# Kernel optimization log

Hardware: AMD Instinct MI355X
Metric: run time of the kernel (lower is better)

Reference implementation:

```python
import jax, jax.numpy as jnp
import numpy as np

NUM_HEADS = 16
WINDOW_SIZE = 256  # config.window_size; layer is 'local'


def setup_inputs() -> dict:
    key = jax.random.key(0)
    ks = jax.random.split(key, 8)
    B, S, H = 4, 2048, 1024
    scale = 1.0 / np.sqrt(H)
    return {
        "x": jax.random.normal(ks[0], (B, S, H), dtype=jnp.float32),
        "x_clean": jax.random.normal(ks[1], (B, S, H), dtype=jnp.float32),
        "ablation_mask": jax.random.uniform(ks[2], (B, S, H), dtype=jnp.float32),
        "Wq": jax.random.normal(ks[3], (H, H), dtype=jnp.float32) * scale,
        "Wk": jax.random.normal(ks[4], (H, H), dtype=jnp.float32) * scale,
        "Wv": jax.random.normal(ks[5], (H, H), dtype=jnp.float32) * scale,
        "Wo": jax.random.normal(ks[6], (H, H), dtype=jnp.float32) * scale,
        "bo": jnp.zeros((H,), dtype=jnp.float32),
    }


def reference(x, x_clean, ablation_mask, Wq, Wk, Wv, Wo, bo):
    B, S, H = x.shape
    nh, hd = NUM_HEADS, H // NUM_HEADS

    def proj(inp, W):  # torch Linear: inp @ W.T -> split heads -> [B, nh, S, hd]
        return jnp.einsum('bsh,oh->bso', inp, W).reshape(B, S, nh, hd).transpose(0, 2, 1, 3)

    q = proj(x, Wq)
    k = proj(x_clean, Wk)
    v = proj(x_clean, Wv)

    # NOTE: original applies NO 1/sqrt(head_dim) scaling.
    scores = jnp.einsum('bnsd,bntd->bnst', q, k)  # [B, nh, S, S]

    i = jnp.arange(S)[:, None]
    j = jnp.arange(S)[None, :]
    # local mask: forbid future (j > i) OR too-far past (j <= i - window)
    masked = (j > i) | (j <= i - WINDOW_SIZE)
    scores = jnp.where(masked[None, None, :, :], -jnp.inf, scores)

    attn = jax.nn.softmax(scores, axis=-1)
    context = jnp.einsum('bnst,bntd->bnsd', attn, v)          # [B, nh, S, hd]
    context = context.transpose(0, 2, 1, 3).reshape(B, S, H)   # merge heads
    context = context * ablation_mask
    return jnp.einsum('bsh,oh->bso', context, Wo) + bo
```

## Files before the change

### kernel.cpp

```cpp
#include <hip/hip_runtime.h>
#include <hip/hip_bf16.h>
#include <cstddef>

#define SB 4
#define SS 2048
#define SH 1024
#define NH 16
#define HD 64
#define WIN 256

typedef __attribute__((ext_vector_type(8))) short bf16x8;
typedef __attribute__((ext_vector_type(8))) _Float16 f16x8;
typedef __attribute__((ext_vector_type(2))) __fp16 fp16v2;
typedef __attribute__((ext_vector_type(4))) float f32x4;

static __device__ __forceinline__ ushort2 pk_bf16(float a, float b) {
    __hip_bfloat162 h = __float22bfloat162_rn(make_float2(a, b));
    union { __hip_bfloat162 h2; ushort2 u2; } u;
    u.h2 = h;
    return u.u2;
}
static __device__ __forceinline__ unsigned short pk1(float a) {
    return pk_bf16(a, 0.f).x;
}

static __device__ __forceinline__ void async16(const void* gptr, void* lptr) {
    __builtin_amdgcn_global_load_lds(
        (const __attribute__((address_space(1))) unsigned int*)gptr,
        (__attribute__((address_space(3))) unsigned int*)lptr, 16, 0, 0);
}

__global__ __launch_bounds__(256) void cvt_all(
    const float* __restrict__ x,  const float* __restrict__ xc,
    const float* __restrict__ Wq, const float* __restrict__ Wk,
    const float* __restrict__ Wv, const float* __restrict__ Wo,
    _Float16* __restrict__ xh,  _Float16* __restrict__ xch,
    _Float16* __restrict__ Wqh, _Float16* __restrict__ Wkh,
    _Float16* __restrict__ Wvh, _Float16* __restrict__ Woh)
{
    const int I4 = SB * SS * SH / 4;
    const int W4 = SH * SH / 4;
    int idx = blockIdx.x * 256 + threadIdx.x;
    const float* src;
    _Float16* dst;
    int off;
    if (idx < I4) { src = x; dst = xh; off = idx; }
    else if (idx < 2 * I4) { src = xc; dst = xch; off = idx - I4; }
    else {
        int r = idx - 2 * I4;
        int wi = r >> 18;
        off = r & (W4 - 1);
        src = (wi == 0) ? Wq : (wi == 1) ? Wk : (wi == 2) ? Wv : Wo;
        dst = (wi == 0) ? Wqh : (wi == 1) ? Wkh : (wi == 2) ? Wvh : Woh;
    }
    float4 v = ((const float4*)src)[off];
    union { fp16v2 h[2]; uint2 u; } t;
    t.h[0] = __builtin_amdgcn_cvt_pkrtz(v.x, v.y);
    t.h[1] = __builtin_amdgcn_cvt_pkrtz(v.z, v.w);
    ((uint2*)dst)[off] = t.u;
}

template<int OUTM>
__global__ __launch_bounds__(256) void gemm5(
    const _Float16* __restrict__ A, const _Float16* __restrict__ W,
    const float* __restrict__ bias, void* __restrict__ C1v,
    int M, int N, int K)
{
    __shared__ __align__(16) unsigned short smem[2 * 128 * 64];
    _Float16* Ah = (_Float16*)smem;
    _Float16* Bh = (_Float16*)smem + 8192;

    const int tid = threadIdx.x;
    const int m0 = blockIdx.x * 128;
    const int n0 = blockIdx.y * 128;
    const int wave = tid >> 6;
    const int lane = tid & 63;
    const int wm = (wave & 1) * 64;
    const int wn = (wave >> 1) * 64;
    const int lrow = lane & 15;
    const int lk8 = (lane >> 4) * 8;
    const int rq = (lane >> 4) * 4;

    f32x4 acc[4][4];
#pragma unroll
    for (int i = 0; i < 4; ++i)
#pragma unroll
        for (int j = 0; j < 4; ++j)
            acc[i][j] = (f32x4){0.f, 0.f, 0.f, 0.f};

    for (int k0 = 0; k0 < K; k0 += 64) {
        __syncthreads();
#pragma unroll
        for (int ki = 0; ki < 2; ++ki)
#pragma unroll
            for (int u = 0; u < 2; ++u) {
                int reg = u * 4 + wave;
                int slot = reg * 64 + lane;
                int row = slot >> 2;
                int k8 = (slot & 3) * 8;
                async16(A + (size_t)(m0 + row) * K + k0 + ki * 32 + k8,
                        Ah + ki * 4096 + reg * 512);
                async16(W + (size_t)(n0 + row) * K + k0 + ki * 32 + k8,
                        Bh + ki * 4096 + reg * 512);
            }
        __syncthreads();

#pragma unroll
        for (int ki = 0; ki < 2; ++ki) {
            f16x8 bf[4];
#pragma unroll
            for (int j = 0; j < 4; ++j)
                bf[j] = *(const f16x8*)&Bh[ki * 4096 + (wn + j * 16 + lrow) * 32 + lk8];
#pragma unroll
            for (int i = 0; i < 4; ++i) {
                f16x8 af = *(const f16x8*)&Ah[ki * 4096 + (wm + i * 16 + lrow) * 32 + lk8];
#pragma unroll
                for (int j = 0; j < 4; ++j)
                    acc[i][j] = __builtin_amdgcn_mfma_f32_16x16x32_f16(af, bf[j], acc[i][j], 0, 0, 0);
            }
        }
    }

    if (OUTM == 0) {
        float* C = (float*)C1v;
#pragma unroll
        for (int i = 0; i < 4; ++i) {
            int rbase = m0 + wm + i * 16 + rq;
#pragma unroll
            for (int j = 0; j < 4; ++j) {
                int col = n0 + wn + j * 16 + lrow;
                float badd = bias[col];
#pragma unroll
                for (int r = 0; r < 4; ++r)
                    C[(size_t)(rbase + r) * N + col] = acc[i][j][r] + badd;
            }
        }
    } else if (OUTM == 1) {
        _Float16* C = (_Float16*)C1v;
#pragma unroll
        for (int i = 0; i < 4; ++i) {
            int rbase = m0 + wm + i * 16 + rq;
#pragma unroll
            for (int j = 0; j < 4; ++j) {
                int col = n0 + wn + j * 16 + lrow;
#pragma unroll
                for (int r = 0; r < 4; ++r)
                    C[(size_t)(rbase + r) * N + col] = (_Float16)acc[i][j][r];
            }
        }
    } else {
        unsigned short* Ct = (unsigned short*)C1v;
        unsigned short* T = smem;
#pragma unroll
        for (int p = 0; p < 2; ++p) {
            __syncthreads();
            if (wn == p * 64) {
#pragma unroll
                for (int i = 0; i < 4; ++i) {
                    int mloc = wm + i * 16 + rq;
#pragma unroll
                    for (int j = 0; j < 4; ++j) {
                        int cl = j * 16 + lrow;
                        *(ushort4*)&T[cl * 136 + mloc] = make_ushort4(
                            pk1(acc[i][j][0]), pk1(acc[i][j][1]),
                            pk1(acc[i][j][2]), pk1(acc[i][j][3]));
                    }
                }
            }
            __syncthreads();
#pragma unroll
            for (int u = 0; u < 4; ++u) {
                int slot = u * 256 + tid;
                int cl = slot >> 4;
                int m8 = (slot & 15) * 8;
                *(uint4*)(Ct + (size_t)(n0 + p * 64 + cl) * M + m0 + m8) =
                    *(const uint4*)&T[cl * 136 + m8];
            }
        }
    }
}

__global__ __launch_bounds__(128) void attn3(
    const _Float16* Qg, const _Float16* __restrict__ Kg,
    const unsigned short* __restrict__ Vtg, const float* __restrict__ amask,
    _Float16* ctxg)
{
    __shared__ __align__(16) unsigned short P_s[2][32 * 72];

    const int t = threadIdx.x;
    const int wave = t >> 6, lane = t & 63;
    const int h = blockIdx.y, b = blockIdx.z;
    const int wq = blockIdx.x * 64 + wave * 32;
    const int lrow = lane & 15;
    const int lk8 = (lane >> 4) * 8;
    const int rq = (lane >> 4) * 4;
    const int M = SB * SS;
    unsigned short* P = P_s[wave];

    f16x8 qf[2][2];
#pragma unroll
    for (int i = 0; i < 2; ++i)
#pragma unroll
        for (int ki = 0; ki < 2; ++ki)
            qf[i][ki] = *(const f16x8*)(Qg +
                (size_t)(b * SS + wq + i * 16 + lrow) * SH + h * HD + ki * 32 + lk8);

    f32x4 o[2][4];
    float lsum[2][4];
#pragma unroll
    for (int i = 0; i < 2; ++i)
#pragma unroll
        for (int j = 0; j < 4; ++j) o[i][j] = (f32x4){0.f, 0.f, 0.f, 0.f};
#pragma unroll
    for (int i = 0; i < 2; ++i)
#pragma unroll
        for (int r = 0; r < 4; ++r) lsum[i][r] = 0.f;

    int cl = wq - (WIN - 1);
    cl = cl < 0 ? 0 : cl;
    const int c_lo = cl >> 6;
    const int c_hi = (wq + 31) >> 6;

    for (int c = c_lo; c <= c_hi; ++c) {
        const int key0 = c * 64;

        f16x8 kf[2][4];
#pragma unroll
        for (int ki = 0; ki < 2; ++ki)
#pragma unroll
            for (int j = 0; j < 4; ++j)
                kf[ki][j] = *(const f16x8*)(Kg +
                    (size_t)(b * SS + key0 + j * 16 + lrow) * SH + h * HD + ki * 32 + lk8);

        f32x4 s[2][4];
#pragma unroll
        for (int i = 0; i < 2; ++i)
#pragma unroll
            for (int j = 0; j < 4; ++j) s[i][j] = (f32x4){0.f, 0.f, 0.f, 0.f};
#pragma unroll
        for (int ki = 0; ki < 2; ++ki)
#pragma unroll
            for (int j = 0; j < 4; ++j)
#pragma unroll
                for (int i = 0; i < 2; ++i)
                    s[i][j] = __builtin_amdgcn_mfma_f32_16x16x32_f16(qf[i][ki], kf[ki][j], s[i][j], 0, 0, 0);

#pragma unroll
        for (int i = 0; i < 2; ++i)
#pragma unroll
            for (int j = 0; j < 4; ++j) {
                int jg = key0 + j * 16 + lrow;
#pragma unroll
                for (int r = 0; r < 4; ++r) {
                    int qg = wq + i * 16 + rq + r;
                    float p = (jg <= qg && jg > qg - WIN) ? __expf(s[i][j][r]) : 0.f;
                    lsum[i][r] += p;
                    P[(i * 16 + rq + r) * 72 + j * 16 + lrow] = pk1(p);
                }
            }

        bf16x8 vf[2][4];
#pragma unroll
        for (int ki = 0; ki < 2; ++ki)
#pragma unroll
            for (int j = 0; j < 4; ++j)
                vf[ki][j] = *(const bf16x8*)(Vtg +
                    (size_t)(h * HD + j * 16 + lrow) * M + b * SS + key0 + ki * 32 + lk8);

#pragma unroll
        for (int ki = 0; ki < 2; ++ki) {
            bf16x8 pf[2];
#pragma unroll
            for (int i = 0; i < 2; ++i)
                pf[i] = *(const bf16x8*)&P[(i * 16 + lrow) * 72 + ki * 32 + lk8];
#pragma unroll
            for (int j = 0; j < 4; ++j)
#pragma unroll
                for (int i = 0; i < 2; ++i)
                    o[i][j] = __builtin_amdgcn_mfma_f32_16x16x32_bf16(pf[i], vf[ki][j], o[i][j], 0, 0, 0);
        }
    }

#pragma unroll
    for (int i = 0; i < 2; ++i)
#pragma unroll
        for (int r = 0; r < 4; ++r) {
#pragma unroll
            for (int m = 1; m < 16; m <<= 1)
                lsum[i][r] += __shfl_xor(lsum[i][r], m);
        }

    _Float16* Pf = (_Float16*)P;
#pragma unroll
    for (int i = 0; i < 2; ++i)
#pragma unroll
        for (int r = 0; r < 4; ++r) {
            float inv = 1.f / lsum[i][r];
#pragma unroll
            for (int j = 0; j < 4; ++j)
                Pf[(i * 16 + rq + r) * 72 + j * 16 + lrow] = (_Float16)(o[i][j][r] * inv);
        }
#pragma unroll
    for (int u = 0; u < 4; ++u) {
        int slot = u * 64 + lane;
        int ro = slot >> 3;
        int d8 = (slot & 7) * 8;
        f16x8 v = *(const f16x8*)&Pf[ro * 72 + d8];
        size_t g = (size_t)(b * SS + wq + ro) * SH + h * HD + d8;
        float4 ma = *(const float4*)(amask + g);
        float4 mb = *(const float4*)(amask + g + 4);
        f16x8 rs;
        rs[0] = (_Float16)((float)v[0] * ma.x);
        rs[1] = (_Float16)((float)v[1] * ma.y);
        rs[2] = (_Float16)((float)v[2] * ma.z);
        rs[3] = (_Float16)((float)v[3] * ma.w);
        rs[4] = (_Float16)((float)v[4] * mb.x);
        rs[5] = (_Float16)((float)v[5] * mb.y);
        rs[6] = (_Float16)((float)v[6] * mb.z);
        rs[7] = (_Float16)((float)v[7] * mb.w);
        *(f16x8*)(ctxg + g) = rs;
    }
}

extern "C" void kernel_launch(void* const* d_in, const int* in_sizes, int n_in,
                              void* d_out, int out_size, void* d_ws, size_t ws_size,
                              hipStream_t stream)
{
    const float* x     = (const float*)d_in[0];
    const float* xc    = (const float*)d_in[1];
    const float* amask = (const float*)d_in[2];
    const float* Wq    = (const float*)d_in[3];
    const float* Wk    = (const float*)d_in[4];
    const float* Wv    = (const float*)d_in[5];
    const float* Wo    = (const float*)d_in[6];
    const float* bo    = (const float*)d_in[7];
    float* out = (float*)d_out;

    const int M = SB * SS;
    const size_t BUF = (size_t)M * SH;
    const size_t WBUF = (size_t)SH * SH;
    _Float16* xh  = (_Float16*)d_ws;
    _Float16* xch = xh + BUF;
    _Float16* Qh  = xch + BUF;
    _Float16* Kh  = Qh + BUF;
    unsigned short* Vt = (unsigned short*)(Kh + BUF);
    _Float16* Wqh = (_Float16*)(Vt + BUF);
    _Float16* Wkh = Wqh + WBUF;
    _Float16* Wvh = Wkh + WBUF;
    _Float16* Woh = Wvh + WBUF;
    _Float16* ctx = Qh;

    const int total4 = 2 * (M * SH / 4) + 4 * (SH * SH / 4);
    hipLaunchKernelGGL(cvt_all, dim3(total4 / 256), dim3(256), 0, stream,
                       x, xc, Wq, Wk, Wv, Wo, xh, xch, Wqh, Wkh, Wvh, Woh);

    dim3 gg(M / 128, SH / 128);
    dim3 gb(256);
    hipLaunchKernelGGL((gemm5<1>), gg, gb, 0, stream, xh,  Wqh, bo, (void*)Qh, M, SH, SH);
    hipLaunchKernelGGL((gemm5<1>), gg, gb, 0, stream, xch, Wkh, bo, (void*)Kh, M, SH, SH);
    hipLaunchKernelGGL((gemm5<2>), gg, gb, 0, stream, xch, Wvh, bo, (void*)Vt, M, SH, SH);

    hipLaunchKernelGGL(attn3, dim3(SS / 64, NH, SB), dim3(128), 0, stream,
                       Qh, Kh, Vt, amask, ctx);

    hipLaunchKernelGGL((gemm5<0>), gg, gb, 0, stream, ctx, Woh, bo, (void*)out, M, SH, SH);
}
```

Measured before the change: 304.4 us.

## Merge QKV projections into one launch and stage K/V tiles through shared memory

The three Q/K/V projection GEMMs become a single launch that uses blockIdx.z to pick inputs and outputs. This removes two launch gaps and lets the three projections share the GPU in one wave. The attention kernel grows to 4 waves covering 128 queries per block, and K and V chunks are loaded with async copies into double-buffered shared memory, so the waves share them instead of each wave reading them from global memory. Each wave skips chunks outside its window, but the per-chunk __syncthreads adds synchronisation, and the larger blocks mean fewer blocks in the grid.

```diff
diff --git a/kernel.cpp b/kernel.cpp
--- a/kernel.cpp
+++ b/kernel.cpp
@@ -60,15 +60,21 @@
     ((uint2*)dst)[off] = t.u;
 }
 
-template<int OUTM>
-__global__ __launch_bounds__(256) void gemm5(
-    const _Float16* __restrict__ A, const _Float16* __restrict__ W,
-    const float* __restrict__ bias, void* __restrict__ C1v,
-    int M, int N, int K)
+__global__ __launch_bounds__(256) void gemm_qkv(
+    const _Float16* __restrict__ xh, const _Float16* __restrict__ xch,
+    const _Float16* __restrict__ Wqh, const _Float16* __restrict__ Wkh,
+    const _Float16* __restrict__ Wvh,
+    _Float16* __restrict__ Qh, _Float16* __restrict__ Kh,
+    unsigned short* __restrict__ Vt)
 {
+    const int M = SB * SS, N = SH, K = SH;
     __shared__ __align__(16) unsigned short smem[2 * 128 * 64];
     _Float16* Ah = (_Float16*)smem;
     _Float16* Bh = (_Float16*)smem + 8192;
+
+    const int z = blockIdx.z;
+    const _Float16* A = (z == 0) ? xh : xch;
+    const _Float16* W = (z == 0) ? Wqh : (z == 1) ? Wkh : Wvh;
 
     const int tid = threadIdx.x;
     const int m0 = blockIdx.x * 128;
@@ -121,35 +127,20 @@
         }
     }
 
-    if (OUTM == 0) {
-        float* C = (float*)C1v;
+    if (z < 2) {
+        _Float16* C = (z == 0) ? Qh : Kh;
 #pragma unroll
         for (int i = 0; i < 4; ++i) {
             int rbase = m0 + wm + i * 16 + rq;
 #pragma unroll
             for (int j = 0; j < 4; ++j) {
                 int col = n0 + wn + j * 16 + lrow;
-                float badd = bias[col];
-#pragma unroll
-                for (int r = 0; r < 4; ++r)
-                    C[(size_t)(rbase + r) * N + col] = acc[i][j][r] + badd;
-            }
-        }
-    } else if (OUTM == 1) {
-        _Float16* C = (_Float16*)C1v;
-#pragma unroll
-        for (int i = 0; i < 4; ++i) {
-            int rbase = m0 + wm + i * 16 + rq;
-#pragma unroll
-            for (int j = 0; j < 4; ++j) {
-                int col = n0 + wn + j * 16 + lrow;
 #pragma unroll
                 for (int r = 0; r < 4; ++r)
                     C[(size_t)(rbase + r) * N + col] = (_Float16)acc[i][j][r];
             }
         }
     } else {
-        unsigned short* Ct = (unsigned short*)C1v;
         unsigned short* T = smem;
 #pragma unroll
         for (int p = 0; p < 2; ++p) {
@@ -173,24 +164,101 @@
                 int slot = u * 256 + tid;
                 int cl = slot >> 4;
                 int m8 = (slot & 15) * 8;
-                *(uint4*)(Ct + (size_t)(n0 + p * 64 + cl) * M + m0 + m8) =
+                *(uint4*)(Vt + (size_t)(n0 + p * 64 + cl) * M + m0 + m8) =
                     *(const uint4*)&T[cl * 136 + m8];
             }
         }
     }
 }
 
-__global__ __launch_bounds__(128) void attn3(
+__global__ __launch_bounds__(256) void gemm_o(
+    const _Float16* __restrict__ A, const _Float16* __restrict__ W,
+    const float* __restrict__ bias, float* __restrict__ C)
+{
+    const int M = SB * SS, N = SH, K = SH;
+    __shared__ __align__(16) unsigned short smem[2 * 128 * 64];
+    _Float16* Ah = (_Float16*)smem;
+    _Float16* Bh = (_Float16*)smem + 8192;
+
+    const int tid = threadIdx.x;
+    const int m0 = blockIdx.x * 128;
+    const int n0 = blockIdx.y * 128;
+    const int wave = tid >> 6;
+    const int lane = tid & 63;
+    const int wm = (wave & 1) * 64;
+    const int wn = (wave >> 1) * 64;
+    const int lrow = lane & 15;
+    const int lk8 = (lane >> 4) * 8;
+    const int rq = (lane >> 4) * 4;
+
+    f32x4 acc[4][4];
+#pragma unroll
+    for (int i = 0; i < 4; ++i)
+#pragma unroll
+        for (int j = 0; j < 4; ++j)
+            acc[i][j] = (f32x4){0.f, 0.f, 0.f, 0.f};
+
+    for (int k0 = 0; k0 < K; k0 += 64) {
+        __syncthreads();
+#pragma unroll
+        for (int ki = 0; ki < 2; ++ki)
+#pragma unroll
+            for (int u = 0; u < 2; ++u) {
+                int reg = u * 4 + wave;
+                int slot = reg * 64 + lane;
+                int row = slot >> 2;
+                int k8 = (slot & 3) * 8;
+                async16(A + (size_t)(m0 + row) * K + k0 + ki * 32 + k8,
+                        Ah + ki * 4096 + reg * 512);
+                async16(W + (size_t)(n0 + row) * K + k0 + ki * 32 + k8,
+                        Bh + ki * 4096 + reg * 512);
+            }
+        __syncthreads();
+
+#pragma unroll
+        for (int ki = 0; ki < 2; ++ki) {
+            f16x8 bf[4];
+#pragma unroll
+            for (int j = 0; j < 4; ++j)
+                bf[j] = *(const f16x8*)&Bh[ki * 4096 + (wn + j * 16 + lrow) * 32 + lk8];
+#pragma unroll
+            for (int i = 0; i < 4; ++i) {
+                f16x8 af = *(const f16x8*)&Ah[ki * 4096 + (wm + i * 16 + lrow) * 32 + lk8];
+#pragma unroll
+                for (int j = 0; j < 4; ++j)
+                    acc[i][j] = __builtin_amdgcn_mfma_f32_16x16x32_f16(af, bf[j], acc[i][j], 0, 0, 0);
+            }
+        }
+    }
+
+#pragma unroll
+    for (int i = 0; i < 4; ++i) {
+        int rbase = m0 + wm + i * 16 + rq;
+#pragma unroll
+        for (int j = 0; j < 4; ++j) {
+            int col = n0 + wn + j * 16 + lrow;
+            float badd = bias[col];
+#pragma unroll
+            for (int r = 0; r < 4; ++r)
+                C[(size_t)(rbase + r) * N + col] = acc[i][j][r] + badd;
+        }
+    }
+}
+
+__global__ __launch_bounds__(256) void attn4(
     const _Float16* Qg, const _Float16* __restrict__ Kg,
     const unsigned short* __restrict__ Vtg, const float* __restrict__ amask,
     _Float16* ctxg)
 {
-    __shared__ __align__(16) unsigned short P_s[2][32 * 72];
+    __shared__ __align__(16) _Float16 K_s[2][2 * 64 * 32];
+    __shared__ __align__(16) unsigned short V_s[2][2 * 64 * 32];
+    __shared__ __align__(16) unsigned short P_s[4][32 * 72];
 
     const int t = threadIdx.x;
     const int wave = t >> 6, lane = t & 63;
-    const int h = blockIdx.y, b = blockIdx.z;
-    const int wq = blockIdx.x * 64 + wave * 32;
+    const int qb = blockIdx.x, h = blockIdx.y, b = blockIdx.z;
+    const int t0 = qb * 128;
+    const int wq = t0 + wave * 32;
     const int lrow = lane & 15;
     const int lk8 = (lane >> 4) * 8;
     const int rq = (lane >> 4) * 4;
@@ -216,69 +284,81 @@
 #pragma unroll
         for (int r = 0; r < 4; ++r) lsum[i][r] = 0.f;
 
-    int cl = wq - (WIN - 1);
-    cl = cl < 0 ? 0 : cl;
-    const int c_lo = cl >> 6;
-    const int c_hi = (wq + 31) >> 6;
+    int cl0 = t0 - (WIN - 1);
+    cl0 = cl0 < 0 ? 0 : cl0;
+    const int c_lo = cl0 >> 6;
+    const int c_hi = (t0 >> 6) + 1;
+
+    auto stage = [&](int c, int buf) {
+        const int key0 = c * 64;
+#pragma unroll
+        for (int ki = 0; ki < 2; ++ki) {
+            int slot = wave * 64 + lane;
+            int row = slot >> 2;
+            int e8 = (slot & 3) * 8;
+            async16(Kg + (size_t)(b * SS + key0 + row) * SH + h * HD + ki * 32 + e8,
+                    (_Float16*)K_s[buf] + ki * 2048 + wave * 512);
+            async16(Vtg + (size_t)(h * HD + row) * M + b * SS + key0 + ki * 32 + e8,
+                    (unsigned short*)V_s[buf] + ki * 2048 + wave * 512);
+        }
+    };
+
+    stage(c_lo, c_lo & 1);
+    __syncthreads();
 
     for (int c = c_lo; c <= c_hi; ++c) {
+        const int cur = c & 1;
+        if (c < c_hi) stage(c + 1, cur ^ 1);
         const int key0 = c * 64;
-
-        f16x8 kf[2][4];
-#pragma unroll
-        for (int ki = 0; ki < 2; ++ki)
-#pragma unroll
-            for (int j = 0; j < 4; ++j)
-                kf[ki][j] = *(const f16x8*)(Kg +
-                    (size_t)(b * SS + key0 + j * 16 + lrow) * SH + h * HD + ki * 32 + lk8);
-
-        f32x4 s[2][4];
-#pragma unroll
-        for (int i = 0; i < 2; ++i)
-#pragma unroll
-            for (int j = 0; j < 4; ++j) s[i][j] = (f32x4){0.f, 0.f, 0.f, 0.f};
-#pragma unroll
-        for (int ki = 0; ki < 2; ++ki)
-#pragma unroll
-            for (int j = 0; j < 4; ++j)
+        if (key0 <= wq + 31 && key0 + 63 >= wq - (WIN - 1)) {
+            const _Float16* Kc = (const _Float16*)K_s[cur];
+            const unsigned short* Vc = (const unsigned short*)V_s[cur];
+
+            f32x4 s[2][4];
+#pragma unroll
+            for (int i = 0; i < 2; ++i)
+#pragma unroll
+                for (int j = 0; j < 4; ++j) s[i][j] = (f32x4){0.f, 0.f, 0.f, 0.f};
+#pragma unroll
+            for (int ki = 0; ki < 2; ++ki)
+#pragma unroll
+                for (int j = 0; j < 4; ++j) {
+                    f16x8 bh = *(const f16x8*)&Kc[ki * 2048 + (j * 16 + lrow) * 32 + lk8];
+#pragma unroll
+                    for (int i = 0; i < 2; ++i)
+                        s[i][j] = __builtin_amdgcn_mfma_f32_16x16x32_f16(qf[i][ki], bh, s[i][j], 0, 0, 0);
+                }
+
+#pragma unroll
+            for (int i = 0; i < 2; ++i)
+#pragma unroll
+                for (int j = 0; j < 4; ++j) {
+                    int jg = key0 + j * 16 + lrow;
+#pragma unroll
+                    for (int r = 0; r < 4; ++r) {
+                        int qg = wq + i * 16 + rq + r;
+                        float p = (jg <= qg && jg > qg - WIN) ? __expf(s[i][j][r]) : 0.f;
+                        lsum[i][r] += p;
+                        P[(i * 16 + rq + r) * 72 + j * 16 + lrow] = pk1(p);
+                    }
+                }
+
+#pragma unroll
+            for (int ki = 0; ki < 2; ++ki) {
+                bf16x8 pf[2];
 #pragma unroll
                 for (int i = 0; i < 2; ++i)
-                    s[i][j] = __builtin_amdgcn_mfma_f32_16x16x32_f16(qf[i][ki], kf[ki][j], s[i][j], 0, 0, 0);
-
-#pragma unroll
-        for (int i = 0; i < 2; ++i)
-#pragma unroll
-            for (int j = 0; j < 4; ++j) {
-                int jg = key0 + j * 16 + lrow;
-#pragma unroll
-                for (int r = 0; r < 4; ++r) {
-                    int qg = wq + i * 16 + rq + r;
-                    float p = (jg <= qg && jg > qg - WIN) ? __expf(s[i][j][r]) : 0.f;
-                    lsum[i][r] += p;
-                    P[(i * 16 + rq + r) * 72 + j * 16 + lrow] = pk1(p);
+                    pf[i] = *(const bf16x8*)&P[(i * 16 + lrow) * 72 + ki * 32 + lk8];
+#pragma unroll
+                for (int j = 0; j < 4; ++j) {
+                    bf16x8 vf = *(const bf16x8*)&Vc[ki * 2048 + (j * 16 + lrow) * 32 + lk8];
+#pragma unroll
+                    for (int i = 0; i < 2; ++i)
+                        o[i][j] = __builtin_amdgcn_mfma_f32_16x16x32_bf16(pf[i], vf, o[i][j], 0, 0, 0);
                 }
             }
-
-        bf16x8 vf[2][4];
-#pragma unroll
-        for (int ki = 0; ki < 2; ++ki)
-#pragma unroll
-            for (int j = 0; j < 4; ++j)
-                vf[ki][j] = *(const bf16x8*)(Vtg +
-                    (size_t)(h * HD + j * 16 + lrow) * M + b * SS + key0 + ki * 32 + lk8);
-
-#pragma unroll
-        for (int ki = 0; ki < 2; ++ki) {
-            bf16x8 pf[2];
-#pragma unroll
-            for (int i = 0; i < 2; ++i)
-                pf[i] = *(const bf16x8*)&P[(i * 16 + lrow) * 72 + ki * 32 + lk8];
-#pragma unroll
-            for (int j = 0; j < 4; ++j)
-#pragma unroll
-                for (int i = 0; i < 2; ++i)
-                    o[i][j] = __builtin_amdgcn_mfma_f32_16x16x32_bf16(pf[i], vf[ki][j], o[i][j], 0, 0, 0);
-        }
+        }
+        __syncthreads();
     }
 
 #pragma unroll
@@ -354,14 +434,12 @@
     hipLaunchKernelGGL(cvt_all, dim3(total4 / 256), dim3(256), 0, stream,
                        x, xc, Wq, Wk, Wv, Wo, xh, xch, Wqh, Wkh, Wvh, Woh);
 
-    dim3 gg(M / 128, SH / 128);
-    dim3 gb(256);
-    hipLaunchKernelGGL((gemm5<1>), gg, gb, 0, stream, xh,  Wqh, bo, (void*)Qh, M, SH, SH);
-    hipLaunchKernelGGL((gemm5<1>), gg, gb, 0, stream, xch, Wkh, bo, (void*)Kh, M, SH, SH);
-    hipLaunchKernelGGL((gemm5<2>), gg, gb, 0, stream, xch, Wvh, bo, (void*)Vt, M, SH, SH);
-
-    hipLaunchKernelGGL(attn3, dim3(SS / 64, NH, SB), dim3(128), 0, stream,
+    hipLaunchKernelGGL(gemm_qkv, dim3(M / 128, SH / 128, 3), dim3(256), 0, stream,
+                       xh, xch, Wqh, Wkh, Wvh, Qh, Kh, Vt);
+
+    hipLaunchKernelGGL(attn4, dim3(SS / 128, NH, SB), dim3(256), 0, stream,
                        Qh, Kh, Vt, amask, ctx);
 
-    hipLaunchKernelGGL((gemm5<0>), gg, gb, 0, stream, ctx, Woh, bo, (void*)out, M, SH, SH);
-}
+    hipLaunchKernelGGL(gemm_o, dim3(M / 128, SH / 128), dim3(256), 0, stream,
+                       ctx, Woh, bo, out);
+}
```

Result: faster. 288.6 us (-5.2%).
